# Performance work log

Hardware: AMD Instinct MI355X
Metric: run time of the kernel (lower is better)

The kernel has to match this reference:

```python
import jax, jax.numpy as jnp
import numpy as np

INF = 1e10  # stand-in for the original global INF constant
D_MODEL = 1024
N_HEADS = 16
SCALE = float(np.sqrt(D_MODEL))  # Attention is built with full d_key, so scale = sqrt(d_model)


def setup_inputs() -> dict:
    key = jax.random.key(0)
    ks = jax.random.split(key, 8)
    B, S, D = 4, 2048, D_MODEL
    s = 1.0 / np.sqrt(D)
    return {
        "query": jax.random.normal(ks[0], (B, S, D), jnp.float32),
        "key": jax.random.normal(ks[1], (B, S, D), jnp.float32),
        "value": jax.random.normal(ks[2], (B, S, D), jnp.float32),
        "wq": jax.random.normal(ks[3], (D, D), jnp.float32) * s,
        "bq": jnp.zeros((D,), jnp.float32),
        "wk": jax.random.normal(ks[4], (D, D), jnp.float32) * s,
        "bk": jnp.zeros((D,), jnp.float32),
        "wv": jax.random.normal(ks[5], (D, D), jnp.float32) * s,
        "bv": jnp.zeros((D,), jnp.float32),
        "wo": jax.random.normal(ks[6], (D, D), jnp.float32) * s,
        "bo": jnp.zeros((D,), jnp.float32),
    }


def reference(query, key, value, wq, bq, wk, bk, wv, bv, wo, bo):
    B, S, D = query.shape
    H = N_HEADS
    dh = D // H
    q = query @ wq + bq
    k = key @ wk + bk
    v = value @ wv + bv
    # split heads: [B, S, H, dh]
    q = q.reshape(B, S, H, dh)
    k = k.reshape(B, S, H, dh)
    v = v.reshape(B, S, H, dh)
    # raw dot products (unscaled), then causal mask subtracted (as in original),
    # then divide by sqrt(d_key) and softmax
    scores = jnp.einsum("bqhd,bkhd->bhqk", q, k)
    causal = jnp.triu(jnp.ones((S, S), scores.dtype), k=1) * INF
    scores = scores - causal  # broadcast over [B, H]
    attn = jax.nn.softmax(scores / SCALE, axis=-1)
    out = jnp.einsum("bhqk,bkhd->bqhd", attn, v).reshape(B, S, D)
    return out @ wo + bo
```

## Files before the change

### kernel.cpp

```cpp
#include <hip/hip_runtime.h>
#include <hip/hip_bf16.h>

typedef __bf16 bf16_t;
typedef __bf16 bf16x8 __attribute__((ext_vector_type(8)));
typedef float f32x4 __attribute__((ext_vector_type(4)));

#define MFMA16(a, b, c) __builtin_amdgcn_mfma_f32_16x16x32_bf16((a), (b), (c), 0, 0, 0)

static constexpr int S_LEN = 2048;
static constexpr int DM = 1024;
static constexpr int NH = 16;
static constexpr int DH = 64;

typedef const __attribute__((address_space(1))) unsigned int gu32;
typedef __attribute__((address_space(3))) unsigned int lu32;
__device__ __forceinline__ void gl_lds16(const void* src, void* dst) {
    __builtin_amdgcn_global_load_lds((gu32*)src, (lu32*)dst, 16, 0, 0);
}

struct PreArgs { const float* w[4]; bf16_t* o[4]; const float* s[3]; bf16_t* d[3]; };

__global__ __launch_bounds__(256) void pre_kernel(PreArgs p) {
    int bid = blockIdx.x;
    int tid = threadIdx.x;
    if (bid < 1024) {
        int wi = bid >> 8;
        int tb = bid & 255;
        int k0 = (tb >> 4) * 64;
        int n0 = (tb & 15) * 64;
        const float* w = p.w[wi];
        bf16_t* o = p.o[wi];
        __shared__ bf16_t t[64 * 66];
#pragma unroll
        for (int i = 0; i < 4; ++i) {
            int f = tid + 256 * i;
            int row = f >> 4;
            int c4 = f & 15;
            f32x4 v = *reinterpret_cast<const f32x4*>(w + (size_t)(k0 + row) * DM + n0 + c4 * 4);
            int base = row * 66 + c4 * 4;
            t[base + 0] = (bf16_t)v[0];
            t[base + 1] = (bf16_t)v[1];
            t[base + 2] = (bf16_t)v[2];
            t[base + 3] = (bf16_t)v[3];
        }
        __syncthreads();
#pragma unroll
        for (int i = 0; i < 2; ++i) {
            int c = tid + 256 * i;
            int n = c >> 3;
            int ck = c & 7;
            union { bf16_t h[8]; uint4 u; } cv;
#pragma unroll
            for (int j = 0; j < 8; ++j) cv.h[j] = t[(ck * 8 + j) * 66 + n];
            *reinterpret_cast<uint4*>(o + (size_t)(n0 + n) * DM + k0 + ck * 8) = cv.u;
        }
    } else {
        int cbid = bid - 1024;
        int ti = cbid >> 12;
        size_t idx = (size_t)(((cbid & 4095) << 8) | tid) * 8;
        const float* s = p.s[ti];
        bf16_t* d = p.d[ti];
        f32x4 v0 = *reinterpret_cast<const f32x4*>(s + idx);
        f32x4 v1 = *reinterpret_cast<const f32x4*>(s + idx + 4);
        union { bf16_t h[8]; uint4 u; } cv;
#pragma unroll
        for (int j = 0; j < 4; ++j) { cv.h[j] = (bf16_t)v0[j]; cv.h[4 + j] = (bf16_t)v1[j]; }
        *reinterpret_cast<uint4*>(d + idx) = cv.u;
    }
}

#define GEMM_CORE(Ab_, BT_)                                                          \
    __shared__ bf16_t a_buf[2][128 * 32];                                            \
    __shared__ bf16_t b_buf[2][128 * 32];                                            \
    f32x4 zero = {0.f, 0.f, 0.f, 0.f};                                               \
    f32x4 acc[4][4];                                                                 \
    _Pragma("unroll") for (int m = 0; m < 4; ++m)                                    \
        _Pragma("unroll") for (int n = 0; n < 4; ++n) acc[m][n] = zero;              \
    int wr = (w >> 1) * 64, wc = (w & 1) * 64;                                       \
    auto stage = [&](int buf, int kt) {                                              \
        int k0 = kt * 32;                                                            \
        _Pragma("unroll") for (int i = 0; i < 2; ++i) {                              \
            int r16 = (w * 2 + i) * 16;                                              \
            int row = r16 + (l >> 2), ch = l & 3;                                    \
            gl_lds16(Ab_ + (size_t)(m0 + row) * 1024 + k0 + ch * 8, &a_buf[buf][r16 * 32]); \
            gl_lds16(BT_ + (size_t)(n0 + row) * 1024 + k0 + ch * 8, &b_buf[buf][r16 * 32]); \
        }                                                                            \
    };                                                                               \
    stage(0, 0);                                                                     \
    int cur = 0;                                                                     \
    for (int kt = 0; kt < 32; ++kt) {                                                \
        __syncthreads();                                                             \
        if (kt + 1 < 32) stage(cur ^ 1, kt + 1);                                     \
        bf16x8 af[4], bfr[4];                                                        \
        _Pragma("unroll") for (int m = 0; m < 4; ++m)                                \
            af[m] = *reinterpret_cast<bf16x8*>(&a_buf[cur][(wr + m * 16 + lc) * 32 + g * 8]); \
        _Pragma("unroll") for (int n = 0; n < 4; ++n)                                \
            bfr[n] = *reinterpret_cast<bf16x8*>(&b_buf[cur][(wc + n * 16 + lc) * 32 + g * 8]); \
        _Pragma("unroll") for (int m = 0; m < 4; ++m)                                \
            _Pragma("unroll") for (int n = 0; n < 4; ++n)                            \
                acc[m][n] = MFMA16(af[m], bfr[n], acc[m][n]);                        \
        cur ^= 1;                                                                    \
    }

struct QKVArgs {
    const bf16_t* A[3]; const bf16_t* BT[3]; const float* bias[3];
    bf16_t* out[3]; float alpha0;
};

__global__ __launch_bounds__(256) void gemm_qkv(QKVArgs a) {
    constexpr int K = 1024;
    int bid = blockIdx.x;
    int wi = bid >> 10;
    int sub = bid & 1023;
    int bm = (sub & 7) * 8 + ((sub >> 3) & 7);
    int bn = sub >> 6;
    int tid = threadIdx.x;
    int w = tid >> 6, l = tid & 63;
    int g = l >> 4, lc = l & 15;

    const bf16_t* Ab = a.A[wi];
    const bf16_t* BT = a.BT[wi];

    __shared__ bf16_t a_buf[2][128 * 32];
    __shared__ bf16_t b_buf[2][64 * 32];

    f32x4 zero = {0.f, 0.f, 0.f, 0.f};
    f32x4 acc[4][2];
#pragma unroll
    for (int m = 0; m < 4; ++m)
#pragma unroll
        for (int n = 0; n < 2; ++n) acc[m][n] = zero;

    int m0 = bm * 128, n0 = bn * 64;
    int wr = (w >> 1) * 64, wc = (w & 1) * 32;

    int scw = (l & 3) ^ ((l >> 3) & 3);
    int fsw = (lc >> 1) & 3;

    auto stage = [&](int buf, int kt) {
        int k0 = kt * 32;
#pragma unroll
        for (int i = 0; i < 2; ++i) {
            int r16 = (w * 2 + i) * 16;
            int row = r16 + (l >> 2);
            gl_lds16(Ab + (size_t)(m0 + row) * K + k0 + scw * 8, &a_buf[buf][r16 * 32]);
        }
        int r16 = w * 16;
        int row = r16 + (l >> 2);
        gl_lds16(BT + (size_t)(n0 + row) * K + k0 + scw * 8, &b_buf[buf][r16 * 32]);
    };

    stage(0, 0);
    int cur = 0;
    for (int kt = 0; kt < K / 32; ++kt) {
        __syncthreads();
        if (kt + 1 < K / 32) stage(cur ^ 1, kt + 1);
        bf16x8 af[4], bfr[2];
#pragma unroll
        for (int m = 0; m < 4; ++m)
            af[m] = *reinterpret_cast<bf16x8*>(
                &a_buf[cur][(wr + m * 16 + lc) * 32 + (g ^ fsw) * 8]);
#pragma unroll
        for (int n = 0; n < 2; ++n)
            bfr[n] = *reinterpret_cast<bf16x8*>(
                &b_buf[cur][(wc + n * 16 + lc) * 32 + (g ^ fsw) * 8]);
#pragma unroll
        for (int m = 0; m < 4; ++m)
#pragma unroll
            for (int n = 0; n < 2; ++n)
                acc[m][n] = MFMA16(af[m], bfr[n], acc[m][n]);
        cur ^= 1;
    }

    float alpha = (wi == 0) ? a.alpha0 : 1.0f;
    const float* bias = a.bias[wi];
    bf16_t* Cp = a.out[wi];
    if (wi == 2) {
#pragma unroll
        for (int n = 0; n < 2; ++n) {
            int ng = n0 + wc + n * 16 + lc;
            float bv = bias[ng];
            int h = ng >> 6, d = ng & 63;
#pragma unroll
            for (int m = 0; m < 4; ++m) {
                int s0g = m0 + wr + m * 16 + g * 4;
                int b = s0g >> 11, s0 = s0g & 2047;
                union { bf16_t hh[4]; uint2 u; } pk;
#pragma unroll
                for (int r = 0; r < 4; ++r)
                    pk.hh[r] = (bf16_t)(acc[m][n][r] + bv);
                *reinterpret_cast<uint2*>(
                    &Cp[(((size_t)(b * NH + h)) * DH + d) * S_LEN + s0]) = pk.u;
            }
        }
    } else {
#pragma unroll
        for (int n = 0; n < 2; ++n) {
            int ng = n0 + wc + n * 16 + lc;
            float bv = bias[ng];
            int h = ng >> 6, d = ng & 63;
#pragma unroll
            for (int m = 0; m < 4; ++m) {
#pragma unroll
                for (int r = 0; r < 4; ++r) {
                    int mg = m0 + wr + m * 16 + g * 4 + r;
                    int b = mg >> 11, s = mg & 2047;
                    Cp[(((size_t)(b * NH + h)) * S_LEN + s) * DH + d] =
                        (bf16_t)((acc[m][n][r] + bv) * alpha);
                }
            }
        }
    }
}

template <int MODE>
__global__ __launch_bounds__(256) void gemm_k(const bf16_t* __restrict__ Ab,
                                              const bf16_t* __restrict__ BT,
                                              const float* __restrict__ bias,
                                              bf16_t* __restrict__ Cp, float alpha) {
    int bid = blockIdx.x;
    int bm = (bid & 7) * 8 + ((bid >> 3) & 7);
    int bn = bid >> 6;
    int tid = threadIdx.x;
    int w = tid >> 6, l = tid & 63;
    int g = l >> 4, lc = l & 15;
    int m0 = bm * 128, n0 = bn * 128;
    GEMM_CORE(Ab, BT)

    if constexpr (MODE == 2) {
#pragma unroll
        for (int n = 0; n < 4; ++n) {
            int ng = n0 + wc + n * 16 + lc;
            float bv = bias[ng];
            int h = ng >> 6, d = ng & 63;
#pragma unroll
            for (int m = 0; m < 4; ++m) {
                int s0g = m0 + wr + m * 16 + g * 4;
                int b = s0g >> 11, s0 = s0g & 2047;
                union { bf16_t hh[4]; uint2 u; } pk;
#pragma unroll
                for (int r = 0; r < 4; ++r)
                    pk.hh[r] = (bf16_t)((acc[m][n][r] + bv) * alpha);
                *reinterpret_cast<uint2*>(
                    &Cp[(((size_t)(b * NH + h)) * DH + d) * S_LEN + s0]) = pk.u;
            }
        }
    } else {
#pragma unroll
        for (int n = 0; n < 4; ++n) {
            int ng = n0 + wc + n * 16 + lc;
            float bv = bias[ng];
            int h = ng >> 6, d = ng & 63;
#pragma unroll
            for (int m = 0; m < 4; ++m) {
#pragma unroll
                for (int r = 0; r < 4; ++r) {
                    int mg = m0 + wr + m * 16 + g * 4 + r;
                    int b = mg >> 11, s = mg & 2047;
                    Cp[(((size_t)(b * NH + h)) * S_LEN + s) * DH + d] =
                        (bf16_t)((acc[m][n][r] + bv) * alpha);
                }
            }
        }
    }
}

__global__ __launch_bounds__(256) void gemm_o(const bf16_t* __restrict__ Ab,
                                              const bf16_t* __restrict__ BT,
                                              const float* __restrict__ bias,
                                              float* __restrict__ Cp) {
    constexpr int K = 1024, N = 1024;
    int bid = blockIdx.x;
    int bm = (bid & 7) * 8 + ((bid >> 3) & 7);
    int bn = bid >> 6;
    int tid = threadIdx.x;
    int w = tid >> 6, l = tid & 63;
    int g = l >> 4, lc = l & 15;

    __shared__ bf16_t a_buf[2][128 * 32];
    __shared__ bf16_t b_buf[2][64 * 32];

    f32x4 zero = {0.f, 0.f, 0.f, 0.f};
    f32x4 acc[4][2];
#pragma unroll
    for (int m = 0; m < 4; ++m)
#pragma unroll
        for (int n = 0; n < 2; ++n) acc[m][n] = zero;

    int m0 = bm * 128, n0 = bn * 64;
    int wr = (w >> 1) * 64, wc = (w & 1) * 32;

    int scw = (l & 3) ^ ((l >> 3) & 3);
    int fsw = (lc >> 1) & 3;

    auto stage = [&](int buf, int kt) {
        int k0 = kt * 32;
#pragma unroll
        for (int i = 0; i < 2; ++i) {
            int r16 = (w * 2 + i) * 16;
            int row = r16 + (l >> 2);
            gl_lds16(Ab + (size_t)(m0 + row) * K + k0 + scw * 8, &a_buf[buf][r16 * 32]);
        }
        int r16 = w * 16;
        int row = r16 + (l >> 2);
        gl_lds16(BT + (size_t)(n0 + row) * K + k0 + scw * 8, &b_buf[buf][r16 * 32]);
    };

    stage(0, 0);
    int cur = 0;
    for (int kt = 0; kt < K / 32; ++kt) {
        __syncthreads();
        if (kt + 1 < K / 32) stage(cur ^ 1, kt + 1);
        bf16x8 af[4], bfr[2];
#pragma unroll
        for (int m = 0; m < 4; ++m)
            af[m] = *reinterpret_cast<bf16x8*>(
                &a_buf[cur][(wr + m * 16 + lc) * 32 + (g ^ fsw) * 8]);
#pragma unroll
        for (int n = 0; n < 2; ++n)
            bfr[n] = *reinterpret_cast<bf16x8*>(
                &b_buf[cur][(wc + n * 16 + lc) * 32 + (g ^ fsw) * 8]);
#pragma unroll
        for (int m = 0; m < 4; ++m)
#pragma unroll
            for (int n = 0; n < 2; ++n)
                acc[m][n] = MFMA16(af[m], bfr[n], acc[m][n]);
        cur ^= 1;
    }

#pragma unroll
    for (int n = 0; n < 2; ++n) {
        int ng = n0 + wc + n * 16 + lc;
        float bv = bias[ng];
#pragma unroll
        for (int m = 0; m < 4; ++m) {
#pragma unroll
            for (int r = 0; r < 4; ++r) {
                int mg = m0 + wr + m * 16 + g * 4 + r;
                Cp[(size_t)mg * N + ng] = acc[m][n][r] + bv;
            }
        }
    }
}

__global__ __launch_bounds__(256) void attn_kernel(const bf16_t* __restrict__ Qh,
                                                   const bf16_t* __restrict__ Kh,
                                                   const bf16_t* __restrict__ Vt,
                                                   bf16_t* __restrict__ AO) {
    int bid = blockIdx.x;
    int qt = 31 - (bid >> 6);
    int bh = bid & 63;
    int h = bh & 15;
    int b = bh >> 4;
    int tid = threadIdx.x;
    int w = tid >> 6, l = tid & 63;
    int g = l >> 4, lc = l & 15;
    int q0 = qt * 64 + w * 16;
    int q = q0 + lc;

    __shared__ bf16_t k_lds[2][64 * 64];
    __shared__ bf16_t v_lds[2][64 * 64];
    __shared__ bf16_t p_lds[4][16 * 64];

    size_t head_off = ((size_t)(b * NH + h)) * S_LEN * DH;

    bf16x8 qf[2];
    {
        const bf16_t* qp = Qh + head_off + (size_t)(q0 + lc) * DH + g * 8;
        qf[0] = *reinterpret_cast<const bf16x8*>(qp);
        qf[1] = *reinterpret_cast<const bf16x8*>(qp + 32);
    }

    const bf16_t* kg0; const bf16_t* kg1; const bf16_t* vg0; const bf16_t* vg1;
    int r8a = w * 16, r8b = w * 16 + 8;
    {
        const bf16_t* Kp = Kh + head_off;
        const bf16_t* Vp = Vt + head_off;
        int rowa = r8a + (l >> 3), rowb = r8b + (l >> 3);
        int sca = (l & 7) ^ (rowa & 7), scb = (l & 7) ^ (rowb & 7);
        kg0 = Kp + (size_t)rowa * DH + sca * 8;
        kg1 = Kp + (size_t)rowb * DH + scb * 8;
        vg0 = Vp + (size_t)rowa * S_LEN + sca * 8;
        vg1 = Vp + (size_t)rowb * S_LEN + scb * 8;
    }

    f32x4 zero = {0.f, 0.f, 0.f, 0.f};
    f32x4 o_acc[4];
#pragma unroll
    for (int nt = 0; nt < 4; ++nt) o_acc[nt] = zero;
    float l_part = 0.f;

    int sw = lc & 7;

    auto stageKV = [&](int buf) {
        gl_lds16(kg0, &k_lds[buf][r8a * 64]);
        gl_lds16(vg0, &v_lds[buf][r8a * 64]);
        gl_lds16(kg1, &k_lds[buf][r8b * 64]);
        gl_lds16(vg1, &v_lds[buf][r8b * 64]);
    };

    stageKV(0);
    int cur = 0;
    for (int t = 0; t <= qt; ++t) {
        int kv0 = t * 64;
        __syncthreads();
        if (t < qt) {
            kg0 += 64 * DH; kg1 += 64 * DH; vg0 += 64; vg1 += 64;
            stageKV(cur ^ 1);
        }

        f32x4 sc[4];
#pragma unroll
        for (int nt = 0; nt < 4; ++nt) {
            int row = nt * 16 + lc;
            bf16x8 kf0 = *reinterpret_cast<bf16x8*>(&k_lds[cur][row * 64 + ((g) ^ sw) * 8]);
            bf16x8 kf1 = *reinterpret_cast<bf16x8*>(&k_lds[cur][row * 64 + ((4 + g) ^ sw) * 8]);
            f32x4 s = zero;
            s = MFMA16(kf0, qf[0], s);
            s = MFMA16(kf1, qf[1], s);
            sc[nt] = s;
        }
        if (t == qt) {
#pragma unroll
            for (int nt = 0; nt < 4; ++nt)
#pragma unroll
                for (int r = 0; r < 4; ++r) {
                    int kv = kv0 + nt * 16 + g * 4 + r;
                    if (kv > q) sc[nt][r] = -1e30f;
                }
        }
#pragma unroll
        for (int nt = 0; nt < 4; ++nt)
#pragma unroll
            for (int r = 0; r < 4; ++r) sc[nt][r] = exp2f(sc[nt][r]);
#pragma unroll
        for (int nt = 0; nt < 4; ++nt)
            l_part += sc[nt][0] + sc[nt][1] + sc[nt][2] + sc[nt][3];
#pragma unroll
        for (int nt = 0; nt < 4; ++nt) {
            union { bf16_t hh[4]; uint2 u; } pk;
#pragma unroll
            for (int r = 0; r < 4; ++r) pk.hh[r] = (bf16_t)sc[nt][r];
            int cu = nt * 2 + (g >> 1);
            *reinterpret_cast<uint2*>(
                &p_lds[w][lc * 64 + ((cu ^ sw) * 8) + (g & 1) * 4]) = pk.u;
        }
        bf16x8 pf0 = *reinterpret_cast<bf16x8*>(&p_lds[w][lc * 64 + ((g) ^ sw) * 8]);
        bf16x8 pf1 = *reinterpret_cast<bf16x8*>(&p_lds[w][lc * 64 + ((4 + g) ^ sw) * 8]);
#pragma unroll
        for (int nt = 0; nt < 4; ++nt) {
            int row = nt * 16 + lc;
            bf16x8 vf0 = *reinterpret_cast<bf16x8*>(&v_lds[cur][row * 64 + ((g) ^ sw) * 8]);
            bf16x8 vf1 = *reinterpret_cast<bf16x8*>(&v_lds[cur][row * 64 + ((4 + g) ^ sw) * 8]);
            o_acc[nt] = MFMA16(pf0, vf0, o_acc[nt]);
            o_acc[nt] = MFMA16(pf1, vf1, o_acc[nt]);
        }
        cur ^= 1;
    }

    float l_s = l_part;
    l_s += __shfl_xor(l_s, 16, 64);
    l_s += __shfl_xor(l_s, 32, 64);

#pragma unroll
    for (int r = 0; r < 4; ++r) {
        float lr = __shfl(l_s, g * 4 + r, 64);
        float inv = 1.0f / lr;
        int qq = q0 + g * 4 + r;
        size_t base = ((size_t)b * S_LEN + qq) * DM + h * DH;
#pragma unroll
        for (int nt = 0; nt < 4; ++nt)
            AO[base + nt * 16 + lc] = (bf16_t)(o_acc[nt][r] * inv);
    }
}

extern "C" void kernel_launch(void* const* d_in, const int* in_sizes, int n_in,
                              void* d_out, int out_size, void* d_ws, size_t ws_size,
                              hipStream_t stream) {
    (void)in_sizes; (void)n_in; (void)out_size;
    const float* query = (const float*)d_in[0];
    const float* key   = (const float*)d_in[1];
    const float* value = (const float*)d_in[2];
    const float* wq = (const float*)d_in[3];
    const float* bq = (const float*)d_in[4];
    const float* wk = (const float*)d_in[5];
    const float* bk = (const float*)d_in[6];
    const float* wv = (const float*)d_in[7];
    const float* bv = (const float*)d_in[8];
    const float* wo = (const float*)d_in[9];
    const float* bo = (const float*)d_in[10];
    float* out = (float*)d_out;

    char* ws = (char*)d_ws;
    const size_t Mi = (size_t)1 << 20;
    bf16_t* wqT = (bf16_t*)(ws + 0 * Mi);
    bf16_t* wkT = (bf16_t*)(ws + 2 * Mi);
    bf16_t* wvT = (bf16_t*)(ws + 4 * Mi);
    bf16_t* woT = (bf16_t*)(ws + 6 * Mi);
    bf16_t* Qh  = (bf16_t*)(ws + 8 * Mi);
    bf16_t* Kh  = (bf16_t*)(ws + 24 * Mi);
    bf16_t* Vt  = (bf16_t*)(ws + 40 * Mi);
    bf16_t* AO  = (bf16_t*)(ws + 56 * Mi);

    const float QALPHA = 0.04508422f;

    bool roomy = (ws_size >= 120 * Mi);
    bf16_t* Xq;
    bf16_t* Xk;
    bf16_t* Xv;
    if (roomy) {
        Xq = (bf16_t*)(ws + 72 * Mi);
        Xk = (bf16_t*)(ws + 88 * Mi);
        Xv = (bf16_t*)(ws + 104 * Mi);
    } else {
        Xq = (bf16_t*)(ws + 24 * Mi);
        Xk = (bf16_t*)(ws + 40 * Mi);
        Xv = (bf16_t*)(ws + 56 * Mi);
    }

    PreArgs p;
    p.w[0] = wq; p.w[1] = wk; p.w[2] = wv; p.w[3] = wo;
    p.o[0] = wqT; p.o[1] = wkT; p.o[2] = wvT; p.o[3] = woT;
    p.s[0] = query; p.s[1] = key; p.s[2] = value;
    p.d[0] = Xq; p.d[1] = Xk; p.d[2] = Xv;
    pre_kernel<<<dim3(1024 + 3 * 4096), dim3(256), 0, stream>>>(p);

    if (roomy) {
        QKVArgs qa;
        qa.A[0] = Xq; qa.A[1] = Xk; qa.A[2] = Xv;
        qa.BT[0] = wqT; qa.BT[1] = wkT; qa.BT[2] = wvT;
        qa.bias[0] = bq; qa.bias[1] = bk; qa.bias[2] = bv;
        qa.out[0] = Qh; qa.out[1] = Kh; qa.out[2] = Vt;
        qa.alpha0 = QALPHA;
        gemm_qkv<<<dim3(3 * 1024), dim3(256), 0, stream>>>(qa);
    } else {
        gemm_k<0><<<dim3(512), dim3(256), 0, stream>>>(Xq, wqT, bq, Qh, QALPHA);
        gemm_k<0><<<dim3(512), dim3(256), 0, stream>>>(Xk, wkT, bk, Kh, 1.0f);
        gemm_k<2><<<dim3(512), dim3(256), 0, stream>>>(Xv, wvT, bv, Vt, 1.0f);
    }

    attn_kernel<<<dim3(2048), dim3(256), 0, stream>>>(Qh, Kh, Vt, AO);

    gemm_o<<<dim3(1024), dim3(256), 0, stream>>>(AO, woT, bo, out);
}
```

Measured before the change: 209.3 us.

## Fuse fp32-to-bf16 activation conversion into QKV GEMM operand loads

The separate pass that converted query/key/value from fp32 to bf16 is removed. The QKV GEMM now streams the fp32 activations directly into LDS through global_load_lds, using a new XOR swizzle, and converts them to bf16 when building the MFMA fragments. This saves a full read-write pass over the activations in global memory. In exchange the A tile in LDS is twice as large, each K step reads twice as many global bytes per A tile, and conversion instructions are added to the inner loop, which may lower occupancy.

Result: no change. 208.7 us (median of 16 runs) (-0.3%).

```diff
diff --git a/kernel.cpp b/kernel.cpp
--- a/kernel.cpp
+++ b/kernel.cpp
@@ -18,92 +18,45 @@
     __builtin_amdgcn_global_load_lds((gu32*)src, (lu32*)dst, 16, 0, 0);
 }
 
-struct PreArgs { const float* w[4]; bf16_t* o[4]; const float* s[3]; bf16_t* d[3]; };
+struct PreArgs { const float* w[4]; bf16_t* o[4]; };
 
 __global__ __launch_bounds__(256) void pre_kernel(PreArgs p) {
     int bid = blockIdx.x;
     int tid = threadIdx.x;
-    if (bid < 1024) {
-        int wi = bid >> 8;
-        int tb = bid & 255;
-        int k0 = (tb >> 4) * 64;
-        int n0 = (tb & 15) * 64;
-        const float* w = p.w[wi];
-        bf16_t* o = p.o[wi];
-        __shared__ bf16_t t[64 * 66];
-#pragma unroll
-        for (int i = 0; i < 4; ++i) {
-            int f = tid + 256 * i;
-            int row = f >> 4;
-            int c4 = f & 15;
-            f32x4 v = *reinterpret_cast<const f32x4*>(w + (size_t)(k0 + row) * DM + n0 + c4 * 4);
-            int base = row * 66 + c4 * 4;
-            t[base + 0] = (bf16_t)v[0];
-            t[base + 1] = (bf16_t)v[1];
-            t[base + 2] = (bf16_t)v[2];
-            t[base + 3] = (bf16_t)v[3];
-        }
-        __syncthreads();
-#pragma unroll
-        for (int i = 0; i < 2; ++i) {
-            int c = tid + 256 * i;
-            int n = c >> 3;
-            int ck = c & 7;
-            union { bf16_t h[8]; uint4 u; } cv;
-#pragma unroll
-            for (int j = 0; j < 8; ++j) cv.h[j] = t[(ck * 8 + j) * 66 + n];
-            *reinterpret_cast<uint4*>(o + (size_t)(n0 + n) * DM + k0 + ck * 8) = cv.u;
-        }
-    } else {
-        int cbid = bid - 1024;
-        int ti = cbid >> 12;
-        size_t idx = (size_t)(((cbid & 4095) << 8) | tid) * 8;
-        const float* s = p.s[ti];
-        bf16_t* d = p.d[ti];
-        f32x4 v0 = *reinterpret_cast<const f32x4*>(s + idx);
-        f32x4 v1 = *reinterpret_cast<const f32x4*>(s + idx + 4);
+    int wi = bid >> 8;
+    int tb = bid & 255;
+    int k0 = (tb >> 4) * 64;
+    int n0 = (tb & 15) * 64;
+    const float* w = p.w[wi];
+    bf16_t* o = p.o[wi];
+    __shared__ bf16_t t[64 * 66];
+#pragma unroll
+    for (int i = 0; i < 4; ++i) {
+        int f = tid + 256 * i;
+        int row = f >> 4;
+        int c4 = f & 15;
+        f32x4 v = *reinterpret_cast<const f32x4*>(w + (size_t)(k0 + row) * DM + n0 + c4 * 4);
+        int base = row * 66 + c4 * 4;
+        t[base + 0] = (bf16_t)v[0];
+        t[base + 1] = (bf16_t)v[1];
+        t[base + 2] = (bf16_t)v[2];
+        t[base + 3] = (bf16_t)v[3];
+    }
+    __syncthreads();
+#pragma unroll
+    for (int i = 0; i < 2; ++i) {
+        int c = tid + 256 * i;
+        int n = c >> 3;
+        int ck = c & 7;
         union { bf16_t h[8]; uint4 u; } cv;
 #pragma unroll
-        for (int j = 0; j < 4; ++j) { cv.h[j] = (bf16_t)v0[j]; cv.h[4 + j] = (bf16_t)v1[j]; }
-        *reinterpret_cast<uint4*>(d + idx) = cv.u;
-    }
-}
-
-#define GEMM_CORE(Ab_, BT_)                                                          \
-    __shared__ bf16_t a_buf[2][128 * 32];                                            \
-    __shared__ bf16_t b_buf[2][128 * 32];                                            \
-    f32x4 zero = {0.f, 0.f, 0.f, 0.f};                                               \
-    f32x4 acc[4][4];                                                                 \
-    _Pragma("unroll") for (int m = 0; m < 4; ++m)                                    \
-        _Pragma("unroll") for (int n = 0; n < 4; ++n) acc[m][n] = zero;              \
-    int wr = (w >> 1) * 64, wc = (w & 1) * 64;                                       \
-    auto stage = [&](int buf, int kt) {                                              \
-        int k0 = kt * 32;                                                            \
-        _Pragma("unroll") for (int i = 0; i < 2; ++i) {                              \
-            int r16 = (w * 2 + i) * 16;                                              \
-            int row = r16 + (l >> 2), ch = l & 3;                                    \
-            gl_lds16(Ab_ + (size_t)(m0 + row) * 1024 + k0 + ch * 8, &a_buf[buf][r16 * 32]); \
-            gl_lds16(BT_ + (size_t)(n0 + row) * 1024 + k0 + ch * 8, &b_buf[buf][r16 * 32]); \
-        }                                                                            \
-    };                                                                               \
-    stage(0, 0);                                                                     \
-    int cur = 0;                                                                     \
-    for (int kt = 0; kt < 32; ++kt) {                                                \
-        __syncthreads();                                                             \
-        if (kt + 1 < 32) stage(cur ^ 1, kt + 1);                                     \
-        bf16x8 af[4], bfr[4];                                                        \
-        _Pragma("unroll") for (int m = 0; m < 4; ++m)                                \
-            af[m] = *reinterpret_cast<bf16x8*>(&a_buf[cur][(wr + m * 16 + lc) * 32 + g * 8]); \
-        _Pragma("unroll") for (int n = 0; n < 4; ++n)                                \
-            bfr[n] = *reinterpret_cast<bf16x8*>(&b_buf[cur][(wc + n * 16 + lc) * 32 + g * 8]); \
-        _Pragma("unroll") for (int m = 0; m < 4; ++m)                                \
-            _Pragma("unroll") for (int n = 0; n < 4; ++n)                            \
-                acc[m][n] = MFMA16(af[m], bfr[n], acc[m][n]);                        \
-        cur ^= 1;                                                                    \
-    }
+        for (int j = 0; j < 8; ++j) cv.h[j] = t[(ck * 8 + j) * 66 + n];
+        *reinterpret_cast<uint4*>(o + (size_t)(n0 + n) * DM + k0 + ck * 8) = cv.u;
+    }
+}
 
 struct QKVArgs {
-    const bf16_t* A[3]; const bf16_t* BT[3]; const float* bias[3];
+    const float* A[3]; const bf16_t* BT[3]; const float* bias[3];
     bf16_t* out[3]; float alpha0;
 };
 
@@ -118,10 +71,10 @@
     int w = tid >> 6, l = tid & 63;
     int g = l >> 4, lc = l & 15;
 
-    const bf16_t* Ab = a.A[wi];
+    const float* Af = a.A[wi];
     const bf16_t* BT = a.BT[wi];
 
-    __shared__ bf16_t a_buf[2][128 * 32];
+    __shared__ float  a_buf[2][128 * 32];
     __shared__ bf16_t b_buf[2][64 * 32];
 
     f32x4 zero = {0.f, 0.f, 0.f, 0.f};
@@ -134,16 +87,18 @@
     int m0 = bm * 128, n0 = bn * 64;
     int wr = (w >> 1) * 64, wc = (w & 1) * 32;
 
+    int sc8 = (l & 7) ^ (l >> 3);
     int scw = (l & 3) ^ ((l >> 3) & 3);
+    int sw8 = lc & 7;
     int fsw = (lc >> 1) & 3;
 
     auto stage = [&](int buf, int kt) {
         int k0 = kt * 32;
 #pragma unroll
-        for (int i = 0; i < 2; ++i) {
-            int r16 = (w * 2 + i) * 16;
-            int row = r16 + (l >> 2);
-            gl_lds16(Ab + (size_t)(m0 + row) * K + k0 + scw * 8, &a_buf[buf][r16 * 32]);
+        for (int i = 0; i < 4; ++i) {
+            int r8 = (w * 4 + i) * 8;
+            int row = r8 + (l >> 3);
+            gl_lds16(Af + (size_t)(m0 + row) * K + k0 + sc8 * 4, &a_buf[buf][r8 * 32]);
         }
         int r16 = w * 16;
         int row = r16 + (l >> 2);
@@ -157,9 +112,15 @@
         if (kt + 1 < K / 32) stage(cur ^ 1, kt + 1);
         bf16x8 af[4], bfr[2];
 #pragma unroll
-        for (int m = 0; m < 4; ++m)
-            af[m] = *reinterpret_cast<bf16x8*>(
-                &a_buf[cur][(wr + m * 16 + lc) * 32 + (g ^ fsw) * 8]);
+        for (int m = 0; m < 4; ++m) {
+            const float* base = &a_buf[cur][(wr + m * 16 + lc) * 32];
+            f32x4 lo = *reinterpret_cast<const f32x4*>(base + (((2 * g) ^ sw8) << 2));
+            f32x4 hi = *reinterpret_cast<const f32x4*>(base + (((2 * g + 1) ^ sw8) << 2));
+            union { bf16_t h[8]; bf16x8 v; } cv;
+#pragma unroll
+            for (int j = 0; j < 4; ++j) { cv.h[j] = (bf16_t)lo[j]; cv.h[4 + j] = (bf16_t)hi[j]; }
+            af[m] = cv.v;
+        }
 #pragma unroll
         for (int n = 0; n < 2; ++n)
             bfr[n] = *reinterpret_cast<bf16x8*>(
@@ -196,58 +157,6 @@
     } else {
 #pragma unroll
         for (int n = 0; n < 2; ++n) {
-            int ng = n0 + wc + n * 16 + lc;
-            float bv = bias[ng];
-            int h = ng >> 6, d = ng & 63;
-#pragma unroll
-            for (int m = 0; m < 4; ++m) {
-#pragma unroll
-                for (int r = 0; r < 4; ++r) {
-                    int mg = m0 + wr + m * 16 + g * 4 + r;
-                    int b = mg >> 11, s = mg & 2047;
-                    Cp[(((size_t)(b * NH + h)) * S_LEN + s) * DH + d] =
-                        (bf16_t)((acc[m][n][r] + bv) * alpha);
-                }
-            }
-        }
-    }
-}
-
-template <int MODE>
-__global__ __launch_bounds__(256) void gemm_k(const bf16_t* __restrict__ Ab,
-                                              const bf16_t* __restrict__ BT,
-                                              const float* __restrict__ bias,
-                                              bf16_t* __restrict__ Cp, float alpha) {
-    int bid = blockIdx.x;
-    int bm = (bid & 7) * 8 + ((bid >> 3) & 7);
-    int bn = bid >> 6;
-    int tid = threadIdx.x;
-    int w = tid >> 6, l = tid & 63;
-    int g = l >> 4, lc = l & 15;
-    int m0 = bm * 128, n0 = bn * 128;
-    GEMM_CORE(Ab, BT)
-
-    if constexpr (MODE == 2) {
-#pragma unroll
-        for (int n = 0; n < 4; ++n) {
-            int ng = n0 + wc + n * 16 + lc;
-            float bv = bias[ng];
-            int h = ng >> 6, d = ng & 63;
-#pragma unroll
-            for (int m = 0; m < 4; ++m) {
-                int s0g = m0 + wr + m * 16 + g * 4;
-                int b = s0g >> 11, s0 = s0g & 2047;
-                union { bf16_t hh[4]; uint2 u; } pk;
-#pragma unroll
-                for (int r = 0; r < 4; ++r)
-                    pk.hh[r] = (bf16_t)((acc[m][n][r] + bv) * alpha);
-                *reinterpret_cast<uint2*>(
-                    &Cp[(((size_t)(b * NH + h)) * DH + d) * S_LEN + s0]) = pk.u;
-            }
-        }
-    } else {
-#pragma unroll
-        for (int n = 0; n < 4; ++n) {
             int ng = n0 + wc + n * 16 + lc;
             float bv = bias[ng];
             int h = ng >> 6, d = ng & 63;
@@ -477,7 +386,7 @@
 extern "C" void kernel_launch(void* const* d_in, const int* in_sizes, int n_in,
                               void* d_out, int out_size, void* d_ws, size_t ws_size,
                               hipStream_t stream) {
-    (void)in_sizes; (void)n_in; (void)out_size;
+    (void)in_sizes; (void)n_in; (void)out_size; (void)ws_size;
     const float* query = (const float*)d_in[0];
     const float* key   = (const float*)d_in[1];
     const float* value = (const float*)d_in[2];
@@ -504,40 +413,18 @@
 
     const float QALPHA = 0.04508422f;
 
-    bool roomy = (ws_size >= 120 * Mi);
-    bf16_t* Xq;
-    bf16_t* Xk;
-    bf16_t* Xv;
-    if (roomy) {
-        Xq = (bf16_t*)(ws + 72 * Mi);
-        Xk = (bf16_t*)(ws + 88 * Mi);
-        Xv = (bf16_t*)(ws + 104 * Mi);
-    } else {
-        Xq = (bf16_t*)(ws + 24 * Mi);
-        Xk = (bf16_t*)(ws + 40 * Mi);
-        Xv = (bf16_t*)(ws + 56 * Mi);
-    }
-
     PreArgs p;
     p.w[0] = wq; p.w[1] = wk; p.w[2] = wv; p.w[3] = wo;
     p.o[0] = wqT; p.o[1] = wkT; p.o[2] = wvT; p.o[3] = woT;
-    p.s[0] = query; p.s[1] = key; p.s[2] = value;
-    p.d[0] = Xq; p.d[1] = Xk; p.d[2] = Xv;
-    pre_kernel<<<dim3(1024 + 3 * 4096), dim3(256), 0, stream>>>(p);
-
-    if (roomy) {
-        QKVArgs qa;
-        qa.A[0] = Xq; qa.A[1] = Xk; qa.A[2] = Xv;
-        qa.BT[0] = wqT; qa.BT[1] = wkT; qa.BT[2] = wvT;
-        qa.bias[0] = bq; qa.bias[1] = bk; qa.bias[2] = bv;
-        qa.out[0] = Qh; qa.out[1] = Kh; qa.out[2] = Vt;
-        qa.alpha0 = QALPHA;
-        gemm_qkv<<<dim3(3 * 1024), dim3(256), 0, stream>>>(qa);
-    } else {
-        gemm_k<0><<<dim3(512), dim3(256), 0, stream>>>(Xq, wqT, bq, Qh, QALPHA);
-        gemm_k<0><<<dim3(512), dim3(256), 0, stream>>>(Xk, wkT, bk, Kh, 1.0f);
-        gemm_k<2><<<dim3(512), dim3(256), 0, stream>>>(Xv, wvT, bv, Vt, 1.0f);
-    }
+    pre_kernel<<<dim3(1024), dim3(256), 0, stream>>>(p);
+
+    QKVArgs qa;
+    qa.A[0] = query; qa.A[1] = key; qa.A[2] = value;
+    qa.BT[0] = wqT; qa.BT[1] = wkT; qa.BT[2] = wvT;
+    qa.bias[0] = bq; qa.bias[1] = bk; qa.bias[2] = bv;
+    qa.out[0] = Qh; qa.out[1] = Kh; qa.out[2] = Vt;
+    qa.alpha0 = QALPHA;
+    gemm_qkv<<<dim3(3 * 1024), dim3(256), 0, stream>>>(qa);
 
     attn_kernel<<<dim3(2048), dim3(256), 0, stream>>>(Qh, Kh, Vt, AO);
 
```
